# Kernel optimization log

Measured on AMD Instinct MI355X. Metric: run time of the kernel, lower is better.

Reference implementation:

```python
import jax, jax.numpy as jnp
import numpy as np

NEG_SLOPE = 0.2


def _gat_conv(x, src, dst, W, a_l, a_r, b, n_nodes, activate):
    """DGL-style GATConv. x:[N,F_in], W:[F_in,H*D], a_l/a_r/b:[H,D]."""
    H, D = a_l.shape
    feat = (x @ W).reshape(n_nodes, H, D)                      # [N,H,D]
    el = jnp.sum(feat * a_l, axis=-1)                          # [N,H]
    er = jnp.sum(feat * a_r, axis=-1)                          # [N,H]
    e = jax.nn.leaky_relu(el[src] + er[dst], NEG_SLOPE)        # [E,H]
    # edge softmax over incoming edges of each dst node (numerically stable)
    emax = jax.ops.segment_max(e, dst, num_segments=n_nodes)   # [N,H]
    emax = jnp.where(jnp.isfinite(emax), emax, 0.0)            # zero-in-degree safe
    ee = jnp.exp(e - emax[dst])                                # [E,H]
    denom = jax.ops.segment_sum(ee, dst, num_segments=n_nodes) # [N,H]
    alpha = ee / jnp.maximum(denom[dst], 1e-9)                 # [E,H]
    # aggregate alpha-weighted src features into dst
    msg = alpha[:, :, None] * feat[src]                        # [E,H,D]
    out = jax.ops.segment_sum(msg, dst, num_segments=n_nodes)  # [N,H,D]
    out = out + b
    if activate:
        out = jax.nn.elu(out)
    return out


def setup_inputs() -> dict:
    key = jax.random.key(0)
    ks = jax.random.split(key, 16)
    N, E, F_in, H, Dh, C = 50000, 800000, 256, 4, 64, 40
    s = lambda fan_in: 1.0 / np.sqrt(fan_in)
    return {
        "x": jax.random.normal(ks[0], (N, F_in), dtype=jnp.float32),
        "edge_index": jax.random.randint(ks[1], (2, E), 0, N, dtype=jnp.int32),
        "W0": jax.random.normal(ks[2], (F_in, H * Dh), dtype=jnp.float32) * s(F_in),
        "al0": jax.random.normal(ks[3], (H, Dh), dtype=jnp.float32) * s(Dh),
        "ar0": jax.random.normal(ks[4], (H, Dh), dtype=jnp.float32) * s(Dh),
        "b0": jnp.zeros((H, Dh), dtype=jnp.float32),
        "W1": jax.random.normal(ks[5], (H * Dh, H * Dh), dtype=jnp.float32) * s(H * Dh),
        "al1": jax.random.normal(ks[6], (H, Dh), dtype=jnp.float32) * s(Dh),
        "ar1": jax.random.normal(ks[7], (H, Dh), dtype=jnp.float32) * s(Dh),
        "b1": jnp.zeros((H, Dh), dtype=jnp.float32),
        "W2": jax.random.normal(ks[8], (H * Dh, H * C), dtype=jnp.float32) * s(H * Dh),
        "al2": jax.random.normal(ks[9], (H, C), dtype=jnp.float32) * s(C),
        "ar2": jax.random.normal(ks[10], (H, C), dtype=jnp.float32) * s(C),
        "b2": jnp.zeros((H, C), dtype=jnp.float32),
    }


def reference(x, edge_index, W0, al0, ar0, b0, W1, al1, ar1, b1, W2, al2, ar2, b2):
    N = x.shape[0]
    src, dst = edge_index[0], edge_index[1]
    h = _gat_conv(x, src, dst, W0, al0, ar0, b0, N, activate=True).reshape(N, -1)
    h = _gat_conv(h, src, dst, W1, al1, ar1, b1, N, activate=True).reshape(N, -1)
    out = _gat_conv(h, src, dst, W2, al2, ar2, b2, N, activate=False)
    logits = out.mean(axis=1)  # mean over heads -> [N, num_classes]
    return logits
```

## Files before the change

kernel.cpp:

```cpp
#include <hip/hip_runtime.h>
#include <hip/hip_bf16.h>
#include <math.h>

#define NEG_SLOPE 0.2f

typedef unsigned short ushortT;
typedef __attribute__((ext_vector_type(8))) short short8;
typedef __attribute__((ext_vector_type(4))) float f32x4;
typedef __attribute__((ext_vector_type(4), aligned(4))) int   int4u;
typedef __attribute__((ext_vector_type(4), aligned(4))) float f4u;

static __device__ __forceinline__ float leaky(float x){ return x > 0.f ? x : NEG_SLOPE * x; }
static __device__ __forceinline__ float elu(float x){ return x > 0.f ? x : (__expf(x) - 1.f); }

static __device__ __forceinline__ ushortT f2bf(float f){
  unsigned u = __float_as_uint(f);
  u += 0x7fff + ((u >> 16) & 1);
  return (ushortT)(u >> 16);
}
static __device__ __forceinline__ float bf2f(ushortT h){ return __uint_as_float((unsigned)h << 16); }
static __device__ __forceinline__ float bf_lo(unsigned u){ return __uint_as_float(u << 16); }
static __device__ __forceinline__ float bf_hi(unsigned u){ return __uint_as_float(u & 0xffff0000u); }


__global__ void hist_kernel(const int* __restrict__ dst, int E, int* __restrict__ counts){
  int i = blockIdx.x*blockDim.x + threadIdx.x;
  if(i < E) atomicAdd(&counts[dst[i]], 1);
}

__global__ void scan1_kernel(const int* __restrict__ counts, int N,
                             int* __restrict__ offsets, int* __restrict__ blocksums){
  __shared__ int sdata[1024];
  int i = blockIdx.x*1024 + threadIdx.x;
  int v = (i<N) ? counts[i] : 0;
  sdata[threadIdx.x] = v;
  __syncthreads();
  for(int off=1; off<1024; off<<=1){
    int t = (threadIdx.x >= off) ? sdata[threadIdx.x-off] : 0;
    __syncthreads();
    sdata[threadIdx.x] += t;
    __syncthreads();
  }
  if(i<N) offsets[i] = sdata[threadIdx.x] - v;
  if(threadIdx.x==1023) blocksums[blockIdx.x] = sdata[1023];
}

__global__ void scan2_kernel(int* __restrict__ blocksums, int nb){
  __shared__ int sdata[64];
  int v = ((int)threadIdx.x < nb) ? blocksums[threadIdx.x] : 0;
  sdata[threadIdx.x] = v;
  __syncthreads();
  for(int off=1; off<64; off<<=1){
    int t = (threadIdx.x >= off) ? sdata[threadIdx.x-off] : 0;
    __syncthreads();
    sdata[threadIdx.x] += t;
    __syncthreads();
  }
  if((int)threadIdx.x < nb) blocksums[threadIdx.x] = sdata[threadIdx.x] - v;
}

__global__ void scan3_kernel(int* __restrict__ offsets, const int* __restrict__ blocksums,
                             int N, int E, int* __restrict__ cursor){
  int i = blockIdx.x*1024 + threadIdx.x;
  if(i < N){
    int o = offsets[i] + blocksums[blockIdx.x];
    offsets[i] = o;
    cursor[i] = o;
  }
  if(i == 0) offsets[N] = E;
}

__global__ void scatter_kernel(const int* __restrict__ src, const int* __restrict__ dst, int E,
                               int* __restrict__ cursor, int* __restrict__ ssrc,
                               int* __restrict__ sdst){
  int i = blockIdx.x*blockDim.x + threadIdx.x;
  if(i < E){
    int d = dst[i];
    int p = atomicAdd(&cursor[d], 1);
    ssrc[p] = src[i];
    sdst[p] = d;
  }
}

__global__ __launch_bounds__(256) void wsplit_pack(const float* __restrict__ W, int N,
                              ushortT* __restrict__ Wh, ushortT* __restrict__ Wl){
  int idx = blockIdx.x*256 + threadIdx.x;
  int lane = idx & 63;
  int t  = (idx >> 6) & 7;
  int nt = idx >> 9;
  int l15 = lane & 15, quad = lane >> 4;
  int n = nt*16 + l15;
  ushortT h[8], l[8];
  #pragma unroll
  for(int j=0;j<8;j++){
    int k = t*32 + quad*8 + j;
    float v = (n < N) ? W[(size_t)k*N + n] : 0.f;
    h[j] = f2bf(v);
    l[j] = f2bf(v - bf2f(h[j]));
  }
  *(short8*)&Wh[(size_t)idx*8] = *(short8*)h;
  *(short8*)&Wl[(size_t)idx*8] = *(short8*)l;
}

__global__ __launch_bounds__(256) void xsplit_pack(const float* __restrict__ x, int M, int Mpad,
                              ushortT* __restrict__ Xh, ushortT* __restrict__ Xl){
  int idx = blockIdx.x*256 + threadIdx.x;
  if(idx >= 8*Mpad) return;
  int t = idx / Mpad, m = idx - t*Mpad;
  size_t base = (size_t)idx * 32;
  if(m < M){
    const float* xr = &x[(size_t)m*256 + t*32];
    #pragma unroll
    for(int c=0;c<4;c++){
      float4 v0 = *(const float4*)&xr[c*8];
      float4 v1 = *(const float4*)&xr[c*8+4];
      float vv[8] = {v0.x,v0.y,v0.z,v0.w,v1.x,v1.y,v1.z,v1.w};
      ushortT h[8], l[8];
      #pragma unroll
      for(int j=0;j<8;j++){
        h[j] = f2bf(vv[j]);
        l[j] = f2bf(vv[j] - bf2f(h[j]));
      }
      *(short8*)&Xh[base + c*8] = *(short8*)h;
      *(short8*)&Xl[base + c*8] = *(short8*)l;
    }
  } else {
    short8 z = {0,0,0,0,0,0,0,0};
    #pragma unroll
    for(int c=0;c<4;c++){ *(short8*)&Xh[base + c*8] = z; *(short8*)&Xl[base + c*8] = z; }
  }
}

__global__ __launch_bounds__(256) void gemm_packed(
    const ushortT* __restrict__ Ah, const ushortT* __restrict__ Al,
    const ushortT* __restrict__ Bh, const ushortT* __restrict__ Bl,
    ushortT* __restrict__ Cm, int M, int Mpad, int N,
    const float* __restrict__ al, const float* __restrict__ ar,
    float* __restrict__ el, float* __restrict__ er){
  const int lane = threadIdx.x & 63;
  const int wv   = threadIdx.x >> 6;
  const int l15  = lane & 15, quad = lane >> 4;
  const int m0   = blockIdx.x*32;
  const int n0   = wv*64;
  const int nt0  = n0 >> 4;

  f32x4 acc[2][4];
  #pragma unroll
  for(int i=0;i<2;i++)
    #pragma unroll
    for(int j=0;j<4;j++){ acc[i][j][0]=0.f; acc[i][j][1]=0.f; acc[i][j][2]=0.f; acc[i][j][3]=0.f; }

  #pragma unroll
  for(int t=0; t<8; t++){
    short8 a_h[2], a_l[2], b_h[4], b_l[4];
    #pragma unroll
    for(int i=0;i<2;i++){
      size_t ad = ((size_t)t*Mpad + (m0 + i*16 + l15))*32 + quad*8;
      a_h[i] = *(const short8*)&Ah[ad];
      a_l[i] = *(const short8*)&Al[ad];
    }
    #pragma unroll
    for(int j=0;j<4;j++){
      size_t bd = (((size_t)(nt0+j)*8 + t)*64 + lane)*8;
      b_h[j] = *(const short8*)&Bh[bd];
      b_l[j] = *(const short8*)&Bl[bd];
    }
    #pragma unroll
    for(int i=0;i<2;i++)
      #pragma unroll
      for(int j=0;j<4;j++){
        acc[i][j] = __builtin_amdgcn_mfma_f32_16x16x32_bf16(a_h[i], b_h[j], acc[i][j], 0,0,0);
        acc[i][j] = __builtin_amdgcn_mfma_f32_16x16x32_bf16(a_h[i], b_l[j], acc[i][j], 0,0,0);
        acc[i][j] = __builtin_amdgcn_mfma_f32_16x16x32_bf16(a_l[i], b_h[j], acc[i][j], 0,0,0);
      }
  }

  if(al){
    const int h = wv;
    float alv[4], arv[4];
    #pragma unroll
    for(int j=0;j<4;j++){
      alv[j] = al[h*64 + j*16 + l15];
      arv[j] = ar[h*64 + j*16 + l15];
    }
    #pragma unroll
    for(int i=0;i<2;i++){
      #pragma unroll
      for(int r=0;r<4;r++){
        float pl = acc[i][0][r]*alv[0] + acc[i][1][r]*alv[1]
                 + acc[i][2][r]*alv[2] + acc[i][3][r]*alv[3];
        float pr = acc[i][0][r]*arv[0] + acc[i][1][r]*arv[1]
                 + acc[i][2][r]*arv[2] + acc[i][3][r]*arv[3];
        #pragma unroll
        for(int off=1; off<16; off<<=1){ pl += __shfl_xor(pl,off); pr += __shfl_xor(pr,off); }
        int gm = m0 + i*16 + quad*4 + r;
        if(l15==0 && gm < M){ el[gm*4+h] = pl; er[gm*4+h] = pr; }
      }
    }
  }

  #pragma unroll
  for(int i=0;i<2;i++){
    #pragma unroll
    for(int r=0;r<4;r++){
      int gm = m0 + i*16 + quad*4 + r;
      if(gm >= M) continue;
      #pragma unroll
      for(int j=0;j<4;j++){
        int gn = n0 + j*16 + l15;
        if(gn < N) Cm[(size_t)gm*N + gn] = f2bf(acc[i][j][r]);
      }
    }
  }
}

__global__ void attn_proj_bf(const __hip_bfloat16* __restrict__ feat, const float* __restrict__ a_l,
                             const float* __restrict__ a_r, float* __restrict__ el,
                             float* __restrict__ er, int D){
  int n = blockIdx.x;
  int h = threadIdx.x >> 6;
  int lane = threadIdx.x & 63;
  float vl = 0.f, vr = 0.f;
  for(int d=lane; d<D; d+=64){
    float f = (float)feat[(size_t)n*4*D + h*D + d];
    vl = fmaf(f, a_l[h*D+d], vl);
    vr = fmaf(f, a_r[h*D+d], vr);
  }
  #pragma unroll
  for(int off=32; off; off>>=1){ vl += __shfl_down(vl,off); vr += __shfl_down(vr,off); }
  if(lane==0){ el[n*4+h] = vl; er[n*4+h] = vr; }
}

__global__ __launch_bounds__(256) void edge_w_kernel(const int* __restrict__ ssrc,
                              const int* __restrict__ sdst, int E,
                              const float4* __restrict__ el4, const float4* __restrict__ er4,
                              float* __restrict__ ewp){
  int e = blockIdx.x*blockDim.x + threadIdx.x;
  if(e >= E) return;
  int s = ssrc[e], d = sdst[e];
  float4 l = el4[s], r = er4[d];
  ewp[e]              = __expf(leaky(l.x + r.x));
  ewp[(size_t)E + e]  = __expf(leaky(l.y + r.y));
  ewp[(size_t)2*E + e]= __expf(leaky(l.z + r.z));
  ewp[(size_t)3*E + e]= __expf(leaky(l.w + r.w));
}

__global__ __launch_bounds__(256) void agg_kernel(const uint4* __restrict__ feat4,
                           const float* __restrict__ ewp,
                           const int* __restrict__ offsets, const int* __restrict__ ssrc,
                           const float* __restrict__ bias,
                           ushortT* __restrict__ Hh, ushortT* __restrict__ Hl,
                           int N, int Mpad, int E){
  int wvi  = threadIdx.x >> 6;
  int lane = threadIdx.x & 63;
  int n = blockIdx.x*4 + wvi;
  if(n >= N) return;
  const int slot = lane >> 5;
  const int wl   = lane & 31;
  const int head = wl >> 3;
  const float* __restrict__ wh = ewp + (size_t)head * E;
  int e0 = offsets[n], e1 = offsets[n+1];
  float a0=0.f,a1=0.f,a2=0.f,a3=0.f,a4=0.f,a5=0.f,a6=0.f,a7=0.f;
  float den = 0.f;
  int e = e0;
  for(; e+7 < e1; e += 8){
    int4u sv = *(const int4u*)&ssrc[e + slot*4];
    f4u   wv = *(const f4u*)  &wh[e + slot*4];
    #pragma unroll
    for(int i=0;i<4;i++){
      uint4 q = feat4[(size_t)sv[i]*32 + wl];
      float w = wv[i];
      a0 = fmaf(w, bf_lo(q.x), a0); a1 = fmaf(w, bf_hi(q.x), a1);
      a2 = fmaf(w, bf_lo(q.y), a2); a3 = fmaf(w, bf_hi(q.y), a3);
      a4 = fmaf(w, bf_lo(q.z), a4); a5 = fmaf(w, bf_hi(q.z), a5);
      a6 = fmaf(w, bf_lo(q.w), a6); a7 = fmaf(w, bf_hi(q.w), a7);
      den += w;
    }
  }
  for(; e < e1; e += 2){
    int ee = e + slot;
    int ec = (ee < e1) ? ee : (e1 - 1);
    float w = (ee < e1) ? wh[ec] : 0.f;
    int s = ssrc[ec];
    uint4 q = feat4[(size_t)s*32 + wl];
    a0 = fmaf(w, bf_lo(q.x), a0); a1 = fmaf(w, bf_hi(q.x), a1);
    a2 = fmaf(w, bf_lo(q.y), a2); a3 = fmaf(w, bf_hi(q.y), a3);
    a4 = fmaf(w, bf_lo(q.z), a4); a5 = fmaf(w, bf_hi(q.z), a5);
    a6 = fmaf(w, bf_lo(q.w), a6); a7 = fmaf(w, bf_hi(q.w), a7);
    den += w;
  }
  a0 += __shfl_xor(a0,32); a1 += __shfl_xor(a1,32);
  a2 += __shfl_xor(a2,32); a3 += __shfl_xor(a3,32);
  a4 += __shfl_xor(a4,32); a5 += __shfl_xor(a5,32);
  a6 += __shfl_xor(a6,32); a7 += __shfl_xor(a7,32);
  den += __shfl_xor(den,32);
  if(slot == 0){
    float inv = 1.f / fmaxf(den, 1e-9f);
    int k0 = wl*8;
    float4 b4a = *(const float4*)&bias[k0];
    float4 b4b = *(const float4*)&bias[k0+4];
    float o[8];
    o[0] = elu(a0*inv + b4a.x); o[1] = elu(a1*inv + b4a.y);
    o[2] = elu(a2*inv + b4a.z); o[3] = elu(a3*inv + b4a.w);
    o[4] = elu(a4*inv + b4b.x); o[5] = elu(a5*inv + b4b.y);
    o[6] = elu(a6*inv + b4b.z); o[7] = elu(a7*inv + b4b.w);
    ushortT hh[8], ll[8];
    #pragma unroll
    for(int j=0;j<8;j++){
      hh[j] = f2bf(o[j]);
      ll[j] = f2bf(o[j] - bf2f(hh[j]));
    }
    int t  = wl >> 2;
    int co = (wl & 3) * 8;
    size_t ad = ((size_t)t*Mpad + n)*32 + co;
    *(short8*)&Hh[ad] = *(short8*)hh;
    *(short8*)&Hl[ad] = *(short8*)ll;
  }
}

__global__ __launch_bounds__(256) void agg2_kernel(const uint2* __restrict__ feat2,
                            const float* __restrict__ ewp,
                            const int* __restrict__ offsets, const int* __restrict__ ssrc,
                            const float* __restrict__ bias, float* __restrict__ logits,
                            int N, int E){
  __shared__ float s_out[4][160];
  int wv = threadIdx.x >> 6;
  int lane = threadIdx.x & 63;
  int n = blockIdx.x*4 + wv;
  bool valid = (n < N);
  if(valid && lane < 40){
    int h = lane / 10;
    const float* __restrict__ wh = ewp + (size_t)h * E;
    int e0 = offsets[n], e1 = offsets[n+1];
    float4 acc0 = make_float4(0.f,0.f,0.f,0.f), acc1 = acc0, acc2 = acc0, acc3 = acc0;
    float den0 = 0.f, den1 = 0.f, den2 = 0.f, den3 = 0.f;
    int e = e0;
    for(; e+3 < e1; e += 4){
      int s0 = ssrc[e], s1 = ssrc[e+1], s2 = ssrc[e+2], s3 = ssrc[e+3];
      float w0 = wh[e];
      float w1 = wh[e+1];
      float w2 = wh[e+2];
      float w3 = wh[e+3];
      uint2 q0 = feat2[(size_t)s0*40 + lane];
      uint2 q1 = feat2[(size_t)s1*40 + lane];
      uint2 q2 = feat2[(size_t)s2*40 + lane];
      uint2 q3 = feat2[(size_t)s3*40 + lane];
      acc0.x = fmaf(w0,bf_lo(q0.x),acc0.x); acc0.y = fmaf(w0,bf_hi(q0.x),acc0.y);
      acc0.z = fmaf(w0,bf_lo(q0.y),acc0.z); acc0.w = fmaf(w0,bf_hi(q0.y),acc0.w); den0 += w0;
      acc1.x = fmaf(w1,bf_lo(q1.x),acc1.x); acc1.y = fmaf(w1,bf_hi(q1.x),acc1.y);
      acc1.z = fmaf(w1,bf_lo(q1.y),acc1.z); acc1.w = fmaf(w1,bf_hi(q1.y),acc1.w); den1 += w1;
      acc2.x = fmaf(w2,bf_lo(q2.x),acc2.x); acc2.y = fmaf(w2,bf_hi(q2.x),acc2.y);
      acc2.z = fmaf(w2,bf_lo(q2.y),acc2.z); acc2.w = fmaf(w2,bf_hi(q2.y),acc2.w); den2 += w2;
      acc3.x = fmaf(w3,bf_lo(q3.x),acc3.x); acc3.y = fmaf(w3,bf_hi(q3.x),acc3.y);
      acc3.z = fmaf(w3,bf_lo(q3.y),acc3.z); acc3.w = fmaf(w3,bf_hi(q3.y),acc3.w); den3 += w3;
    }
    for(; e < e1; e++){
      int s = ssrc[e];
      float w = wh[e];
      uint2 q = feat2[(size_t)s*40 + lane];
      acc0.x = fmaf(w,bf_lo(q.x),acc0.x); acc0.y = fmaf(w,bf_hi(q.x),acc0.y);
      acc0.z = fmaf(w,bf_lo(q.y),acc0.z); acc0.w = fmaf(w,bf_hi(q.y),acc0.w); den0 += w;
    }
    float denom = (den0+den1) + (den2+den3);
    float4 acc;
    acc.x = (acc0.x+acc1.x) + (acc2.x+acc3.x);
    acc.y = (acc0.y+acc1.y) + (acc2.y+acc3.y);
    acc.z = (acc0.z+acc1.z) + (acc2.z+acc3.z);
    acc.w = (acc0.w+acc1.w) + (acc2.w+acc3.w);
    float inv = 1.f / fmaxf(denom, 1e-9f);
    float4 b4 = *(const float4*)&bias[lane*4];
    s_out[wv][lane*4+0] = acc.x*inv + b4.x;
    s_out[wv][lane*4+1] = acc.y*inv + b4.y;
    s_out[wv][lane*4+2] = acc.z*inv + b4.z;
    s_out[wv][lane*4+3] = acc.w*inv + b4.w;
  }
  __syncthreads();
  if(valid && lane < 40){
    logits[(size_t)n*40 + lane] =
        0.25f * (s_out[wv][lane] + s_out[wv][40+lane] + s_out[wv][80+lane] + s_out[wv][120+lane]);
  }
}

extern "C" void kernel_launch(void* const* d_in, const int* in_sizes, int n_in,
                              void* d_out, int out_size, void* d_ws, size_t ws_size,
                              hipStream_t stream){
  const float* x   = (const float*)d_in[0];
  const int*   eix = (const int*)  d_in[1];
  const float* W0  = (const float*)d_in[2];
  const float* al0 = (const float*)d_in[3];
  const float* ar0 = (const float*)d_in[4];
  const float* b0  = (const float*)d_in[5];
  const float* W1  = (const float*)d_in[6];
  const float* al1 = (const float*)d_in[7];
  const float* ar1 = (const float*)d_in[8];
  const float* b1  = (const float*)d_in[9];
  const float* W2  = (const float*)d_in[10];
  const float* al2 = (const float*)d_in[11];
  const float* ar2 = (const float*)d_in[12];
  const float* b2  = (const float*)d_in[13];
  float* logits = (float*)d_out;

  const int N = in_sizes[0] / 256;
  const int E = in_sizes[1] / 2;
  const int* src = eix;
  const int* dst = eix + E;
  const int nb = (N + 1023) / 1024;

  char* ws = (char*)d_ws;
  auto alloc = [&](size_t bytes)->char*{
    char* p = ws; ws += (bytes + 255) & ~(size_t)255; return p;
  };
  const int nblocksM = (N + 127)/128;
  const int Mpad = nblocksM * 128;
  const size_t apackElems = (size_t)Mpad * 256;
  int*   counts    = (int*)  alloc((size_t)N*4);
  int*   offsets   = (int*)  alloc((size_t)(N+1)*4);
  int*   cursor    = (int*)  alloc((size_t)N*4);
  int*   blocksums = (int*)  alloc((size_t)nb*4);
  int*   ssrc      = (int*)  alloc((size_t)E*4);
  int*   sdst      = (int*)  alloc((size_t)E*4);
  float* ew        = (float*)alloc((size_t)E*4*4);
  __hip_bfloat16* bufF = (__hip_bfloat16*)alloc((size_t)N*256*2);
  ushortT* Hh      = (ushortT*)alloc(apackElems*2);
  ushortT* Hl      = (ushortT*)alloc(apackElems*2);
  float* el_buf    = (float*)alloc((size_t)N*4*4);
  float* er_buf    = (float*)alloc((size_t)N*4*4);
  ushortT* Wph0 = (ushortT*)alloc(16*8*64*8*2);
  ushortT* Wpl0 = (ushortT*)alloc(16*8*64*8*2);
  ushortT* Wph1 = (ushortT*)alloc(16*8*64*8*2);
  ushortT* Wpl1 = (ushortT*)alloc(16*8*64*8*2);
  ushortT* Wph2 = (ushortT*)alloc(16*8*64*8*2);
  ushortT* Wpl2 = (ushortT*)alloc(16*8*64*8*2);

  hipMemsetAsync(counts, 0, (size_t)N*4, stream);
  hist_kernel   <<<(E+255)/256, 256, 0, stream>>>(dst, E, counts);
  scan1_kernel  <<<nb, 1024, 0, stream>>>(counts, N, offsets, blocksums);
  scan2_kernel  <<<1, 64, 0, stream>>>(blocksums, nb);
  scan3_kernel  <<<nb, 1024, 0, stream>>>(offsets, blocksums, N, E, cursor);
  scatter_kernel<<<(E+255)/256, 256, 0, stream>>>(src, dst, E, cursor, ssrc, sdst);

  wsplit_pack<<<32, 256, 0, stream>>>(W0, 256, Wph0, Wpl0);
  wsplit_pack<<<32, 256, 0, stream>>>(W1, 256, Wph1, Wpl1);
  wsplit_pack<<<32, 256, 0, stream>>>(W2, 160, Wph2, Wpl2);
  int xtotal = 8 * Mpad;
  xsplit_pack<<<(xtotal+255)/256, 256, 0, stream>>>(x, N, Mpad, Hh, Hl);

  int ggBlocks = Mpad / 32;
  int aggGrid  = (N+3)/4;
  int ewGrid  = (E+255)/256;
  gemm_packed<<<ggBlocks, 256, 0, stream>>>(Hh, Hl, Wph0, Wpl0, (ushortT*)bufF, N, Mpad, 256, al0, ar0, el_buf, er_buf);
  edge_w_kernel<<<ewGrid, 256, 0, stream>>>(ssrc, sdst, E, (const float4*)el_buf, (const float4*)er_buf, ew);
  agg_kernel<<<aggGrid, 256, 0, stream>>>((const uint4*)bufF, ew, offsets, ssrc, b0, Hh, Hl, N, Mpad, E);
  gemm_packed<<<ggBlocks, 256, 0, stream>>>(Hh, Hl, Wph1, Wpl1, (ushortT*)bufF, N, Mpad, 256, al1, ar1, el_buf, er_buf);
  edge_w_kernel<<<ewGrid, 256, 0, stream>>>(ssrc, sdst, E, (const float4*)el_buf, (const float4*)er_buf, ew);
  agg_kernel<<<aggGrid, 256, 0, stream>>>((const uint4*)bufF, ew, offsets, ssrc, b1, Hh, Hl, N, Mpad, E);
  gemm_packed<<<ggBlocks, 256, 0, stream>>>(Hh, Hl, Wph2, Wpl2, (ushortT*)bufF, N, Mpad, 160, nullptr, nullptr, nullptr, nullptr);
  attn_proj_bf<<<N, 256, 0, stream>>>(bufF, al2, ar2, el_buf, er_buf, 40);
  edge_w_kernel<<<ewGrid, 256, 0, stream>>>(ssrc, sdst, E, (const float4*)el_buf, (const float4*)er_buf, ew);
  agg2_kernel<<<aggGrid, 256, 0, stream>>>((const uint2*)bufF, ew, offsets, ssrc, b2, logits, N, E);
}
```

Baseline: 566.8 us.

## Fuse edge-weight computation into aggregation kernels and drop sorted dst array

Removes the separate edge_w_kernel and its E x 4 weight buffer; each aggregation kernel now recomputes exp(leaky(el[src]+er[dst])) inline from the per-node el/er arrays. This also drops the sdst array written by the scatter. It trades an extra global write+read of edge weights and three kernel launches for redundant exp work across lanes and an extra gathered el load per edge. Softmax still skips the max subtraction, as before.

Result: faster. 545.9 us (-3.7%).

```diff
diff --git a/kernel.cpp b/kernel.cpp
--- a/kernel.cpp
+++ b/kernel.cpp
@@ -8,7 +8,6 @@
 typedef __attribute__((ext_vector_type(8))) short short8;
 typedef __attribute__((ext_vector_type(4))) float f32x4;
 typedef __attribute__((ext_vector_type(4), aligned(4))) int   int4u;
-typedef __attribute__((ext_vector_type(4), aligned(4))) float f4u;
 
 static __device__ __forceinline__ float leaky(float x){ return x > 0.f ? x : NEG_SLOPE * x; }
 static __device__ __forceinline__ float elu(float x){ return x > 0.f ? x : (__expf(x) - 1.f); }
@@ -71,14 +70,12 @@
 }
 
 __global__ void scatter_kernel(const int* __restrict__ src, const int* __restrict__ dst, int E,
-                               int* __restrict__ cursor, int* __restrict__ ssrc,
-                               int* __restrict__ sdst){
+                               int* __restrict__ cursor, int* __restrict__ ssrc){
   int i = blockIdx.x*blockDim.x + threadIdx.x;
   if(i < E){
     int d = dst[i];
     int p = atomicAdd(&cursor[d], 1);
     ssrc[p] = src[i];
-    sdst[p] = d;
   }
 }
 
@@ -231,26 +228,12 @@
   if(lane==0){ el[n*4+h] = vl; er[n*4+h] = vr; }
 }
 
-__global__ __launch_bounds__(256) void edge_w_kernel(const int* __restrict__ ssrc,
-                              const int* __restrict__ sdst, int E,
-                              const float4* __restrict__ el4, const float4* __restrict__ er4,
-                              float* __restrict__ ewp){
-  int e = blockIdx.x*blockDim.x + threadIdx.x;
-  if(e >= E) return;
-  int s = ssrc[e], d = sdst[e];
-  float4 l = el4[s], r = er4[d];
-  ewp[e]              = __expf(leaky(l.x + r.x));
-  ewp[(size_t)E + e]  = __expf(leaky(l.y + r.y));
-  ewp[(size_t)2*E + e]= __expf(leaky(l.z + r.z));
-  ewp[(size_t)3*E + e]= __expf(leaky(l.w + r.w));
-}
-
 __global__ __launch_bounds__(256) void agg_kernel(const uint4* __restrict__ feat4,
-                           const float* __restrict__ ewp,
+                           const float* __restrict__ el, const float* __restrict__ er,
                            const int* __restrict__ offsets, const int* __restrict__ ssrc,
                            const float* __restrict__ bias,
                            ushortT* __restrict__ Hh, ushortT* __restrict__ Hl,
-                           int N, int Mpad, int E){
+                           int N, int Mpad){
   int wvi  = threadIdx.x >> 6;
   int lane = threadIdx.x & 63;
   int n = blockIdx.x*4 + wvi;
@@ -258,18 +241,18 @@
   const int slot = lane >> 5;
   const int wl   = lane & 31;
   const int head = wl >> 3;
-  const float* __restrict__ wh = ewp + (size_t)head * E;
+  const float ern = er[n*4 + head];
   int e0 = offsets[n], e1 = offsets[n+1];
   float a0=0.f,a1=0.f,a2=0.f,a3=0.f,a4=0.f,a5=0.f,a6=0.f,a7=0.f;
   float den = 0.f;
   int e = e0;
   for(; e+7 < e1; e += 8){
     int4u sv = *(const int4u*)&ssrc[e + slot*4];
-    f4u   wv = *(const f4u*)  &wh[e + slot*4];
     #pragma unroll
     for(int i=0;i<4;i++){
-      uint4 q = feat4[(size_t)sv[i]*32 + wl];
-      float w = wv[i];
+      int s = sv[i];
+      float w = __expf(leaky(el[s*4 + head] + ern));
+      uint4 q = feat4[(size_t)s*32 + wl];
       a0 = fmaf(w, bf_lo(q.x), a0); a1 = fmaf(w, bf_hi(q.x), a1);
       a2 = fmaf(w, bf_lo(q.y), a2); a3 = fmaf(w, bf_hi(q.y), a3);
       a4 = fmaf(w, bf_lo(q.z), a4); a5 = fmaf(w, bf_hi(q.z), a5);
@@ -280,8 +263,8 @@
   for(; e < e1; e += 2){
     int ee = e + slot;
     int ec = (ee < e1) ? ee : (e1 - 1);
-    float w = (ee < e1) ? wh[ec] : 0.f;
     int s = ssrc[ec];
+    float w = (ee < e1) ? __expf(leaky(el[s*4 + head] + ern)) : 0.f;
     uint4 q = feat4[(size_t)s*32 + wl];
     a0 = fmaf(w, bf_lo(q.x), a0); a1 = fmaf(w, bf_hi(q.x), a1);
     a2 = fmaf(w, bf_lo(q.y), a2); a3 = fmaf(w, bf_hi(q.y), a3);
@@ -319,10 +302,10 @@
 }
 
 __global__ __launch_bounds__(256) void agg2_kernel(const uint2* __restrict__ feat2,
-                            const float* __restrict__ ewp,
+                            const float* __restrict__ el, const float* __restrict__ er,
                             const int* __restrict__ offsets, const int* __restrict__ ssrc,
                             const float* __restrict__ bias, float* __restrict__ logits,
-                            int N, int E){
+                            int N){
   __shared__ float s_out[4][160];
   int wv = threadIdx.x >> 6;
   int lane = threadIdx.x & 63;
@@ -330,17 +313,17 @@
   bool valid = (n < N);
   if(valid && lane < 40){
     int h = lane / 10;
-    const float* __restrict__ wh = ewp + (size_t)h * E;
+    const float ern = er[n*4 + h];
     int e0 = offsets[n], e1 = offsets[n+1];
     float4 acc0 = make_float4(0.f,0.f,0.f,0.f), acc1 = acc0, acc2 = acc0, acc3 = acc0;
     float den0 = 0.f, den1 = 0.f, den2 = 0.f, den3 = 0.f;
     int e = e0;
     for(; e+3 < e1; e += 4){
       int s0 = ssrc[e], s1 = ssrc[e+1], s2 = ssrc[e+2], s3 = ssrc[e+3];
-      float w0 = wh[e];
-      float w1 = wh[e+1];
-      float w2 = wh[e+2];
-      float w3 = wh[e+3];
+      float w0 = __expf(leaky(el[s0*4 + h] + ern));
+      float w1 = __expf(leaky(el[s1*4 + h] + ern));
+      float w2 = __expf(leaky(el[s2*4 + h] + ern));
+      float w3 = __expf(leaky(el[s3*4 + h] + ern));
       uint2 q0 = feat2[(size_t)s0*40 + lane];
       uint2 q1 = feat2[(size_t)s1*40 + lane];
       uint2 q2 = feat2[(size_t)s2*40 + lane];
@@ -356,7 +339,7 @@
     }
     for(; e < e1; e++){
       int s = ssrc[e];
-      float w = wh[e];
+      float w = __expf(leaky(el[s*4 + h] + ern));
       uint2 q = feat2[(size_t)s*40 + lane];
       acc0.x = fmaf(w,bf_lo(q.x),acc0.x); acc0.y = fmaf(w,bf_hi(q.x),acc0.y);
       acc0.z = fmaf(w,bf_lo(q.y),acc0.z); acc0.w = fmaf(w,bf_hi(q.y),acc0.w); den0 += w;
@@ -418,8 +401,6 @@
   int*   cursor    = (int*)  alloc((size_t)N*4);
   int*   blocksums = (int*)  alloc((size_t)nb*4);
   int*   ssrc      = (int*)  alloc((size_t)E*4);
-  int*   sdst      = (int*)  alloc((size_t)E*4);
-  float* ew        = (float*)alloc((size_t)E*4*4);
   __hip_bfloat16* bufF = (__hip_bfloat16*)alloc((size_t)N*256*2);
   ushortT* Hh      = (ushortT*)alloc(apackElems*2);
   ushortT* Hl      = (ushortT*)alloc(apackElems*2);
@@ -437,7 +418,7 @@
   scan1_kernel  <<<nb, 1024, 0, stream>>>(counts, N, offsets, blocksums);
   scan2_kernel  <<<1, 64, 0, stream>>>(blocksums, nb);
   scan3_kernel  <<<nb, 1024, 0, stream>>>(offsets, blocksums, N, E, cursor);
-  scatter_kernel<<<(E+255)/256, 256, 0, stream>>>(src, dst, E, cursor, ssrc, sdst);
+  scatter_kernel<<<(E+255)/256, 256, 0, stream>>>(src, dst, E, cursor, ssrc);
 
   wsplit_pack<<<32, 256, 0, stream>>>(W0, 256, Wph0, Wpl0);
   wsplit_pack<<<32, 256, 0, stream>>>(W1, 256, Wph1, Wpl1);
@@ -447,15 +428,11 @@
 
   int ggBlocks = Mpad / 32;
   int aggGrid  = (N+3)/4;
-  int ewGrid  = (E+255)/256;
   gemm_packed<<<ggBlocks, 256, 0, stream>>>(Hh, Hl, Wph0, Wpl0, (ushortT*)bufF, N, Mpad, 256, al0, ar0, el_buf, er_buf);
-  edge_w_kernel<<<ewGrid, 256, 0, stream>>>(ssrc, sdst, E, (const float4*)el_buf, (const float4*)er_buf, ew);
-  agg_kernel<<<aggGrid, 256, 0, stream>>>((const uint4*)bufF, ew, offsets, ssrc, b0, Hh, Hl, N, Mpad, E);
+  agg_kernel<<<aggGrid, 256, 0, stream>>>((const uint4*)bufF, el_buf, er_buf, offsets, ssrc, b0, Hh, Hl, N, Mpad);
   gemm_packed<<<ggBlocks, 256, 0, stream>>>(Hh, Hl, Wph1, Wpl1, (ushortT*)bufF, N, Mpad, 256, al1, ar1, el_buf, er_buf);
-  edge_w_kernel<<<ewGrid, 256, 0, stream>>>(ssrc, sdst, E, (const float4*)el_buf, (const float4*)er_buf, ew);
-  agg_kernel<<<aggGrid, 256, 0, stream>>>((const uint4*)bufF, ew, offsets, ssrc, b1, Hh, Hl, N, Mpad, E);
+  agg_kernel<<<aggGrid, 256, 0, stream>>>((const uint4*)bufF, el_buf, er_buf, offsets, ssrc, b1, Hh, Hl, N, Mpad);
   gemm_packed<<<ggBlocks, 256, 0, stream>>>(Hh, Hl, Wph2, Wpl2, (ushortT*)bufF, N, Mpad, 160, nullptr, nullptr, nullptr, nullptr);
   attn_proj_bf<<<N, 256, 0, stream>>>(bufF, al2, ar2, el_buf, er_buf, 40);
-  edge_w_kernel<<<ewGrid, 256, 0, stream>>>(ssrc, sdst, E, (const float4*)el_buf, (const float4*)er_buf, ew);
-  agg2_kernel<<<aggGrid, 256, 0, stream>>>((const uint2*)bufF, ew, offsets, ssrc, b2, logits, N, E);
-}
+  agg2_kernel<<<aggGrid, 256, 0, stream>>>((const uint2*)bufF, el_buf, er_buf, offsets, ssrc, b2, logits, N);
+}
```
